# Kernel optimization log

Measured on AMD Instinct MI355X. Metric: run time of the kernel, lower is better.

Reference implementation:

```python
import jax, jax.numpy as jnp
import numpy as np

TOPK_FALLBACK = 12  # hard-coded k in the torch source


def setup_inputs() -> dict:
    key = jax.random.key(0)
    k1, k2 = jax.random.split(key)
    bs, C, H, W = 16, 256, 128, 128
    feature_q = jax.random.normal(k1, (bs, C, H, W), dtype=jnp.float32)
    out = jax.random.normal(k2, (bs, 2, H, W), dtype=jnp.float32)
    tau = jnp.asarray(0.5, dtype=jnp.float32)  # learned threshold parameter
    return {"feature_q": feature_q, "out": out, "tau": tau}


def _proto(feat, p, thres):
    # feat: [bs, C, N], p: [bs, N] probabilities, thres: scalar
    mask = (p > thres).astype(feat.dtype)            # [bs, N]
    cnt = mask.sum(axis=-1)                          # [bs]
    # masked mean over spatial positions (single fused reduction pass)
    masked_mean = jnp.einsum('bcn,bn->bc', feat, mask) / jnp.maximum(cnt, 1.0)[:, None]
    # branchless top-k fallback when no position passes the threshold
    _, idx = jax.lax.top_k(p, TOPK_FALLBACK)         # [bs, k]
    topk_mean = jnp.take_along_axis(feat, idx[:, None, :], axis=2).mean(axis=-1)  # [bs, C]
    return jnp.where((cnt > 0)[:, None], masked_mean, topk_mean)


def reference(feature_q, out, tau):
    bs, C = feature_q.shape[0], feature_q.shape[1]
    pred = jax.nn.softmax(out.reshape(bs, 2, -1), axis=1)  # [bs, 2, N]
    pred_fg, pred_bg = pred[:, 1], pred[:, 0]
    feat = feature_q.reshape(bs, C, -1)                    # [bs, C, N]
    fg_thres = jax.nn.sigmoid(tau)
    bg_thres = 1.0 - fg_thres
    fg_proto = _proto(feat, pred_fg, fg_thres)[:, :, None, None]  # [bs, C, 1, 1]
    bg_proto = _proto(feat, pred_bg, bg_thres)[:, :, None, None]
    return fg_proto, bg_proto
```

## Files before the change

### kernel.cpp

```cpp
#include <hip/hip_runtime.h>
#include <math.h>
#include <stdint.h>

#define BS   16
#define CH   256
#define NPIX 16384
#define TOPK 12
#define WPB  (NPIX / 64)

typedef float nfloat4 __attribute__((ext_vector_type(4)));

__global__ __launch_bounds__(256) void mask_kernel(
    const float* __restrict__ outp,
    const float* __restrict__ tau,
    uint64_t* __restrict__ mfg,
    uint64_t* __restrict__ mbg)
{
    int b = blockIdx.x >> 6;
    int n = ((blockIdx.x & 63) << 8) + threadIdx.x;

    float t = tau[0];
    float fthres = 1.0f / (1.0f + expf(-t));
    float bthres = 1.0f - fthres;

    float o0 = outp[((size_t)b * 2    ) * NPIX + n];
    float o1 = outp[((size_t)b * 2 + 1) * NPIX + n];
    float m  = fmaxf(o0, o1);
    float e0 = expf(o0 - m);
    float e1 = expf(o1 - m);
    float inv = 1.0f / (e0 + e1);

    int fg = (e1 * inv) > fthres;
    int bg = (e0 * inv) > bthres;

    uint64_t bf = __ballot(fg);
    uint64_t bb = __ballot(bg);
    if ((threadIdx.x & 63) == 0) {
        int w = n >> 6;
        mfg[b * WPB + w] = bf;
        mbg[b * WPB + w] = bb;
    }
}

__global__ __launch_bounds__(256) void sum_kernel(
    const float* __restrict__ feat,
    const uint64_t* __restrict__ mfg,
    const uint64_t* __restrict__ mbg,
    float* __restrict__ dout)
{
    int b = blockIdx.x >> 8;
    int c = blockIdx.x & (CH - 1);

    __shared__ uint64_t lf[WPB], lb[WPB];
    lf[threadIdx.x] = mfg[b * WPB + threadIdx.x];
    lb[threadIdx.x] = mbg[b * WPB + threadIdx.x];
    __syncthreads();

    const nfloat4* fp = (const nfloat4*)(feat + (((size_t)b * CH + c) << 14));

    float sfg = 0.0f, sbg = 0.0f;
    #pragma unroll
    for (int i = 0; i < 16; ++i) {
        int idx = i * 256 + threadIdx.x;
        nfloat4 f = __builtin_nontemporal_load(&fp[idx]);
        int p = idx << 2;
        unsigned fb = (unsigned)(lf[p >> 6] >> (p & 63)) & 0xF;
        unsigned bb = (unsigned)(lb[p >> 6] >> (p & 63)) & 0xF;
        if (fb & 1) sfg += f.x;
        if (fb & 2) sfg += f.y;
        if (fb & 4) sfg += f.z;
        if (fb & 8) sfg += f.w;
        if (bb & 1) sbg += f.x;
        if (bb & 2) sbg += f.y;
        if (bb & 4) sbg += f.z;
        if (bb & 8) sbg += f.w;
    }

    #pragma unroll
    for (int off = 32; off > 0; off >>= 1) {
        sfg += __shfl_down(sfg, off);
        sbg += __shfl_down(sbg, off);
    }
    __shared__ float shf[4], shb[4];
    int lane = threadIdx.x & 63, wid = threadIdx.x >> 6;
    if (lane == 0) { shf[wid] = sfg; shb[wid] = sbg; }
    __syncthreads();
    if (threadIdx.x == 0) {
        dout[b * CH + c]           = shf[0] + shf[1] + shf[2] + shf[3];
        dout[BS * CH + b * CH + c] = shb[0] + shb[1] + shb[2] + shb[3];
    }
}

__global__ __launch_bounds__(256) void finalize_kernel(
    const float* __restrict__ feat,
    const float* __restrict__ outp,
    const uint64_t* __restrict__ mfg,
    const uint64_t* __restrict__ mbg,
    float* __restrict__ dout)
{
    int b     = blockIdx.x >> 1;
    int which = blockIdx.x & 1;
    const uint64_t* mw = which ? mbg : mfg;
    float* o = dout + (size_t)which * BS * CH + (size_t)b * CH;

    int pc = (int)__popcll(mw[b * WPB + threadIdx.x]);
    #pragma unroll
    for (int off = 32; off > 0; off >>= 1) pc += __shfl_down(pc, off);
    __shared__ int sw[4];
    if ((threadIdx.x & 63) == 0) sw[threadIdx.x >> 6] = pc;
    __syncthreads();
    int cnt = sw[0] + sw[1] + sw[2] + sw[3];

    if (cnt > 0) {
        o[threadIdx.x] = o[threadIdx.x] / (float)cnt;
        return;
    }

    __shared__ int   sel[TOPK];
    __shared__ float shv[256];
    __shared__ int   shi[256];

    const float* o0p = outp + ((size_t)b * 2) * NPIX;
    const float* o1p = o0p + NPIX;

    for (int k = 0; k < TOPK; ++k) {
        float bestv = -INFINITY;
        int   besti = 0x7fffffff;
        for (int n = threadIdx.x; n < NPIX; n += 256) {
            bool skip = false;
            for (int j = 0; j < k; ++j) if (sel[j] == n) { skip = true; break; }
            if (skip) continue;
            float a0 = o0p[n], a1 = o1p[n];
            float m  = fmaxf(a0, a1);
            float e0 = expf(a0 - m);
            float e1 = expf(a1 - m);
            float p  = (which == 0 ? e1 : e0) / (e0 + e1);
            if (p > bestv || (p == bestv && n < besti)) { bestv = p; besti = n; }
        }
        shv[threadIdx.x] = bestv;
        shi[threadIdx.x] = besti;
        __syncthreads();
        for (int off = 128; off > 0; off >>= 1) {
            if (threadIdx.x < off) {
                float v2 = shv[threadIdx.x + off];
                int   i2 = shi[threadIdx.x + off];
                if (v2 > shv[threadIdx.x] ||
                    (v2 == shv[threadIdx.x] && i2 < shi[threadIdx.x])) {
                    shv[threadIdx.x] = v2;
                    shi[threadIdx.x] = i2;
                }
            }
            __syncthreads();
        }
        if (threadIdx.x == 0) sel[k] = shi[0];
        __syncthreads();
    }

    const float* fb = feat + ((size_t)b * CH + threadIdx.x) * (size_t)NPIX;
    float s = 0.0f;
    for (int j = 0; j < TOPK; ++j) s += fb[sel[j]];
    o[threadIdx.x] = s / (float)TOPK;
}

extern "C" void kernel_launch(void* const* d_in, const int* in_sizes, int n_in,
                              void* d_out, int out_size, void* d_ws, size_t ws_size,
                              hipStream_t stream) {
    const float* feat = (const float*)d_in[0];
    const float* outp = (const float*)d_in[1];
    const float* tau  = (const float*)d_in[2];
    float* dout = (float*)d_out;

    uint64_t* mfg = (uint64_t*)d_ws;
    uint64_t* mbg = (uint64_t*)((char*)d_ws + (size_t)BS * WPB * 8);

    mask_kernel<<<BS * (NPIX / 256), 256, 0, stream>>>(outp, tau, mfg, mbg);
    sum_kernel<<<BS * CH, 256, 0, stream>>>(feat, mfg, mbg, dout);
    finalize_kernel<<<2 * BS, 256, 0, stream>>>(feat, outp, mfg, mbg, dout);
}
```

Before: 336.8 us.

## Restructure masked sum into persistent grid-stride blocks with scratch partials and reduce pass

Replaces the one-block-per-(batch,channel) masked sum with 2048 blocks that stride over the whole feature tensor, each wave reducing its 256-float4 chunk and writing a per-row partial into a scratch buffer. A new reduce kernel then sums the 64 partials per row into the output. The goal is fewer, longer-lived blocks with more loads in flight to better saturate HBM bandwidth. In exchange it adds a kernel launch, a scratch round-trip, a wave reduction on every iteration, and mask reads from global memory instead of LDS.

```diff
diff --git a/kernel.cpp b/kernel.cpp
--- a/kernel.cpp
+++ b/kernel.cpp
@@ -7,6 +7,8 @@
 #define NPIX 16384
 #define TOPK 12
 #define WPB  (NPIX / 64)
+#define NBLK 2048
+#define NITER 32
 
 typedef float nfloat4 __attribute__((ext_vector_type(4)));
 
@@ -46,48 +48,63 @@
     const float* __restrict__ feat,
     const uint64_t* __restrict__ mfg,
     const uint64_t* __restrict__ mbg,
+    float* __restrict__ scratch)
+{
+    const int tid  = threadIdx.x;
+    const int lane = tid & 63;
+    const int wid  = tid >> 6;
+    const int slot = ((blockIdx.x & 15) << 2) | wid;
+
+    const nfloat4* fp = (const nfloat4*)feat;
+
+    #pragma unroll 4
+    for (int k = 0; k < NITER; ++k) {
+        unsigned i = ((unsigned)(k * NBLK + blockIdx.x) << 8) | (unsigned)tid;
+        nfloat4 f = __builtin_nontemporal_load(&fp[i]);
+
+        unsigned b    = i >> 20;
+        unsigned word = (i & 4095u) >> 4;
+        unsigned midx = (b << 8) | word;
+        uint64_t wf = mfg[midx];
+        uint64_t wb = mbg[midx];
+        unsigned sh = (i & 15u) << 2;
+        unsigned fb = (unsigned)(wf >> sh) & 0xF;
+        unsigned bb = (unsigned)(wb >> sh) & 0xF;
+
+        float sfg = 0.f, sbg = 0.f;
+        sfg += (fb & 1) ? f.x : 0.f;
+        sfg += (fb & 2) ? f.y : 0.f;
+        sfg += (fb & 4) ? f.z : 0.f;
+        sfg += (fb & 8) ? f.w : 0.f;
+        sbg += (bb & 1) ? f.x : 0.f;
+        sbg += (bb & 2) ? f.y : 0.f;
+        sbg += (bb & 4) ? f.z : 0.f;
+        sbg += (bb & 8) ? f.w : 0.f;
+
+        #pragma unroll
+        for (int off = 32; off > 0; off >>= 1) {
+            sfg += __shfl_down(sfg, off);
+            sbg += __shfl_down(sbg, off);
+        }
+        if (lane == 0) {
+            unsigned row = i >> 12;
+            scratch[(row << 6) | slot]                 = sfg;
+            scratch[(4096u << 6) + ((row << 6) | slot)] = sbg;
+        }
+    }
+}
+
+__global__ __launch_bounds__(256) void reduce_kernel(
+    const float* __restrict__ scratch,
     float* __restrict__ dout)
 {
-    int b = blockIdx.x >> 8;
-    int c = blockIdx.x & (CH - 1);
-
-    __shared__ uint64_t lf[WPB], lb[WPB];
-    lf[threadIdx.x] = mfg[b * WPB + threadIdx.x];
-    lb[threadIdx.x] = mbg[b * WPB + threadIdx.x];
-    __syncthreads();
-
-    const nfloat4* fp = (const nfloat4*)(feat + (((size_t)b * CH + c) << 14));
-
-    float sfg = 0.0f, sbg = 0.0f;
-    #pragma unroll
-    for (int i = 0; i < 16; ++i) {
-        int idx = i * 256 + threadIdx.x;
-        nfloat4 f = __builtin_nontemporal_load(&fp[idx]);
-        int p = idx << 2;
-        unsigned fb = (unsigned)(lf[p >> 6] >> (p & 63)) & 0xF;
-        unsigned bb = (unsigned)(lb[p >> 6] >> (p & 63)) & 0xF;
-        if (fb & 1) sfg += f.x;
-        if (fb & 2) sfg += f.y;
-        if (fb & 4) sfg += f.z;
-        if (fb & 8) sfg += f.w;
-        if (bb & 1) sbg += f.x;
-        if (bb & 2) sbg += f.y;
-        if (bb & 4) sbg += f.z;
-        if (bb & 8) sbg += f.w;
-    }
-
-    #pragma unroll
-    for (int off = 32; off > 0; off >>= 1) {
-        sfg += __shfl_down(sfg, off);
-        sbg += __shfl_down(sbg, off);
-    }
-    __shared__ float shf[4], shb[4];
-    int lane = threadIdx.x & 63, wid = threadIdx.x >> 6;
-    if (lane == 0) { shf[wid] = sfg; shb[wid] = sbg; }
-    __syncthreads();
-    if (threadIdx.x == 0) {
-        dout[b * CH + c]           = shf[0] + shf[1] + shf[2] + shf[3];
-        dout[BS * CH + b * CH + c] = shb[0] + shb[1] + shb[2] + shb[3];
+    int lane = threadIdx.x & 63;
+    int wave = (blockIdx.x << 2) | (threadIdx.x >> 6);
+    for (int v = wave; v < 2 * 4096; v += 512) {
+        float s = scratch[((unsigned)v << 6) | lane];
+        #pragma unroll
+        for (int off = 32; off > 0; off >>= 1) s += __shfl_down(s, off);
+        if (lane == 0) dout[v] = s;
     }
 }
 
@@ -172,8 +189,10 @@
 
     uint64_t* mfg = (uint64_t*)d_ws;
     uint64_t* mbg = (uint64_t*)((char*)d_ws + (size_t)BS * WPB * 8);
+    float* scratch = (float*)((char*)d_ws + 2 * (size_t)BS * WPB * 8);
 
     mask_kernel<<<BS * (NPIX / 256), 256, 0, stream>>>(outp, tau, mfg, mbg);
-    sum_kernel<<<BS * CH, 256, 0, stream>>>(feat, mfg, mbg, dout);
+    sum_kernel<<<NBLK, 256, 0, stream>>>(feat, mfg, mbg, scratch);
+    reduce_kernel<<<128, 256, 0, stream>>>(scratch, dout);
     finalize_kernel<<<2 * BS, 256, 0, stream>>>(feat, outp, mfg, mbg, dout);
 }
```

After: 358.1 us. 1.06x slower.
